# Kernel optimization log

Hardware: AMD Instinct MI355X
Metric: run time of the kernel (lower is better)

## Reference

```python
import jax, jax.numpy as jnp
import numpy as np

B, K, C = 512, 64, 2048  # batch, mixture components, copy (eval points)


def setup_inputs() -> dict:
    key = jax.random.key(0)
    kw, km, ks, kr, kx = jax.random.split(key, 5)
    w = jax.random.uniform(kw, (B, K), dtype=jnp.float32)            # mixture weights
    means = jax.random.normal(km, (B, K, 2), dtype=jnp.float32)      # mean1, mean2
    sds = jax.random.uniform(ks, (B, K, 2), dtype=jnp.float32,
                             minval=0.5, maxval=1.5)                 # sd1, sd2 (>0)
    corr = jax.random.uniform(kr, (B, K), dtype=jnp.float32,
                              minval=-0.8, maxval=0.8)               # |corr| < 1
    model_out = jnp.concatenate(
        [w[..., None], means, sds, corr[..., None]], axis=-1)        # [B, K, 6]
    X = jax.random.normal(kx, (B, C, 2), dtype=jnp.float32)
    return {"model_out": model_out, "X": X}


def reference(model_out, X):
    # Unpack params: w, mean1, mean2, sd1, sd2, corr  -- each [B, K]
    w = model_out[..., 0]
    m1 = model_out[..., 1]
    m2 = model_out[..., 2]
    s1 = model_out[..., 3]
    s2 = model_out[..., 4]
    r = model_out[..., 5]

    # Closed-form bivariate normal pdf (equivalent to Cholesky-based
    # MultivariateNormal log_prob for the 2x2 covariance built in torch).
    # dx, dy: [B, C, K] via broadcasting X[B,C,1] against params[B,1,K]
    dx = (X[:, :, 0:1] - m1[:, None, :]) / s1[:, None, :]
    dy = (X[:, :, 1:2] - m2[:, None, :]) / s2[:, None, :]
    rb = r[:, None, :]
    omr2 = 1.0 - rb * rb  # 1 - rho^2
    z = dx * dx - 2.0 * rb * dx * dy + dy * dy
    two_pi = 2.0 * jnp.pi
    norm = two_pi * s1[:, None, :] * s2[:, None, :] * jnp.sqrt(omr2)
    probs = jnp.exp(-0.5 * z / omr2) / norm  # [B, C, K]

    # Weighted sum over components -> [B, C]
    return jnp.einsum('bck,bk->bc', probs, w)
```

## Files before the change

### kernel.cpp

```cpp
#include <hip/hip_runtime.h>
#include <hip/hip_bf16.h>


typedef float v2f __attribute__((ext_vector_type(2)));

constexpr int B = 512;
constexpr int K = 64;
constexpr int C = 2048;
constexpr int BLOCK = 256;
constexpr int HALVES = 2;
constexpr int CH = C / HALVES;

__global__ __launch_bounds__(BLOCK, 4) void mixture_kernel(
    const float* __restrict__ mo,
    const float* __restrict__ X,
    float* __restrict__ out)
{
    __shared__ float4 P[K][2];

    const int bid = blockIdx.x;
    const int b   = bid >> 1;
    const int h   = bid & 1;
    const int t   = threadIdx.x;

    if (t < K) {
        const float* p = mo + ((size_t)(b * K + t)) * 6;
        const float w  = p[0];
        const float m1 = p[1];
        const float m2 = p[2];
        const float s1 = p[3];
        const float s2 = p[4];
        const float r  = p[5];

        const float omr2 = fmaf(-r, r, 1.0f);
        const float inv  = 1.0f / omr2;
        const float a2   = 0.7213475204444817f * inv;
        const float sc   = sqrtf(a2);
        const float is1  = sc / s1;
        const float is2  = sc / s2;
        const float wn   = w * 0.15915494309189535f / (s1 * s2 * sqrtf(omr2));

        P[t][0] = make_float4(is1, is2, m1 * is1, m2 * is2);
        P[t][1] = make_float4(2.0f * r, wn, 0.0f, 0.0f);
    }
    __syncthreads();

    const float4* Xb = (const float4*)(X + (size_t)b * C * 2 + (size_t)h * CH * 2);
    const float4 xv0 = Xb[t];
    const float4 xv1 = Xb[t + BLOCK];

    v2f xs[2] = { {xv0.x, xv0.z}, {xv1.x, xv1.z} };
    v2f ys[2] = { {xv0.y, xv0.w}, {xv1.y, xv1.w} };
    v2f acc[2] = { {0.0f, 0.0f}, {0.0f, 0.0f} };

#pragma unroll 4
    for (int k = 0; k < K; ++k) {
        const float4 p0 = P[k][0];
        const float4 p1 = P[k][1];
        const v2f vis1 = { p0.x, p0.x };
        const v2f vis2 = { p0.y, p0.y };
        const v2f vnm1 = { -p0.z, -p0.z };
        const v2f vnm2 = { -p0.w, -p0.w };
        const v2f v2r  = { p1.x, p1.x };
        const v2f vwn  = { p1.y, p1.y };
#pragma unroll
        for (int j = 0; j < 2; ++j) {
            const v2f dx = __builtin_elementwise_fma(xs[j], vis1, vnm1);
            const v2f dy = __builtin_elementwise_fma(ys[j], vis2, vnm2);
            const v2f pq = dx * dy;
            v2f u        = dx * dx;
            u            = __builtin_elementwise_fma(dy, dy, u);
            const v2f e  = __builtin_elementwise_fma(v2r, pq, -u);
            v2f ex;
            ex.x = __builtin_amdgcn_exp2f(e.x);
            ex.y = __builtin_amdgcn_exp2f(e.y);
            acc[j] = __builtin_elementwise_fma(vwn, ex, acc[j]);
        }
    }

    float2* ob = (float2*)(out + (size_t)b * C + (size_t)h * CH);
    ob[t]         = make_float2(acc[0].x, acc[0].y);
    ob[t + BLOCK] = make_float2(acc[1].x, acc[1].y);
}

extern "C" void kernel_launch(void* const* d_in, const int* in_sizes, int n_in,
                              void* d_out, int out_size, void* d_ws, size_t ws_size,
                              hipStream_t stream) {
    const float* mo = (const float*)d_in[0];
    const float* X  = (const float*)d_in[1];
    float* out      = (float*)d_out;

    mixture_kernel<<<dim3(B * HALVES), dim3(BLOCK), 0, stream>>>(mo, X, out);
}
```

Baseline: 72.35 us.

## Split parameter preprocessing into separate prep kernel with pre-broadcast layout

```diff
diff --git a/kernel.cpp b/kernel.cpp
--- a/kernel.cpp
+++ b/kernel.cpp
@@ -11,76 +11,97 @@
 constexpr int HALVES = 2;
 constexpr int CH = C / HALVES;
 
-__global__ __launch_bounds__(BLOCK, 4) void mixture_kernel(
+__global__ __launch_bounds__(256) void prep_kernel(
     const float* __restrict__ mo,
+    float* __restrict__ P)
+{
+    const int i = blockIdx.x * 256 + threadIdx.x;
+    const float* p = mo + (size_t)i * 6;
+    const float w  = p[0];
+    const float m1 = p[1];
+    const float m2 = p[2];
+    const float s1 = p[3];
+    const float s2 = p[4];
+    const float r  = p[5];
+
+    const float omr2 = fmaf(-r, r, 1.0f);
+    const float inv  = 1.0f / omr2;
+    const float a2   = 0.7213475204444817f * inv;
+    const float sc   = sqrtf(a2);
+    const float is1  = sc / s1;
+    const float is2  = sc / s2;
+    const float nm1  = -(m1 * is1);
+    const float nm2  = -(m2 * is2);
+    const float r2   = 2.0f * r;
+    const float wn   = w * 0.15915494309189535f / (s1 * s2 * sqrtf(omr2));
+
+    float4* q = (float4*)(P + (size_t)i * 16);
+    q[0] = make_float4(is1, is1, is2, is2);
+    q[1] = make_float4(nm1, nm1, nm2, nm2);
+    q[2] = make_float4(r2, r2, wn, wn);
+}
+
+__global__ __launch_bounds__(BLOCK) void mixture_kernel(
     const float* __restrict__ X,
+    const float* __restrict__ P,
     float* __restrict__ out)
 {
-    __shared__ float4 P[K][2];
-
     const int bid = blockIdx.x;
     const int b   = bid >> 1;
     const int h   = bid & 1;
     const int t   = threadIdx.x;
 
-    if (t < K) {
-        const float* p = mo + ((size_t)(b * K + t)) * 6;
-        const float w  = p[0];
-        const float m1 = p[1];
-        const float m2 = p[2];
-        const float s1 = p[3];
-        const float s2 = p[4];
-        const float r  = p[5];
-
-        const float omr2 = fmaf(-r, r, 1.0f);
-        const float inv  = 1.0f / omr2;
-        const float a2   = 0.7213475204444817f * inv;
-        const float sc   = sqrtf(a2);
-        const float is1  = sc / s1;
-        const float is2  = sc / s2;
-        const float wn   = w * 0.15915494309189535f / (s1 * s2 * sqrtf(omr2));
-
-        P[t][0] = make_float4(is1, is2, m1 * is1, m2 * is2);
-        P[t][1] = make_float4(2.0f * r, wn, 0.0f, 0.0f);
-    }
-    __syncthreads();
-
     const float4* Xb = (const float4*)(X + (size_t)b * C * 2 + (size_t)h * CH * 2);
     const float4 xv0 = Xb[t];
     const float4 xv1 = Xb[t + BLOCK];
 
-    v2f xs[2] = { {xv0.x, xv0.z}, {xv1.x, xv1.z} };
-    v2f ys[2] = { {xv0.y, xv0.w}, {xv1.y, xv1.w} };
-    v2f acc[2] = { {0.0f, 0.0f}, {0.0f, 0.0f} };
+    const v2f xs0 = { xv0.x, xv0.z };
+    const v2f ys0 = { xv0.y, xv0.w };
+    const v2f xs1 = { xv1.x, xv1.z };
+    const v2f ys1 = { xv1.y, xv1.w };
+    v2f acc0 = { 0.0f, 0.0f };
+    v2f acc1 = { 0.0f, 0.0f };
+
+    const v2f* __restrict__ Pb = (const v2f*)(P + (size_t)b * K * 16);
 
 #pragma unroll 4
     for (int k = 0; k < K; ++k) {
-        const float4 p0 = P[k][0];
-        const float4 p1 = P[k][1];
-        const v2f vis1 = { p0.x, p0.x };
-        const v2f vis2 = { p0.y, p0.y };
-        const v2f vnm1 = { -p0.z, -p0.z };
-        const v2f vnm2 = { -p0.w, -p0.w };
-        const v2f v2r  = { p1.x, p1.x };
-        const v2f vwn  = { p1.y, p1.y };
-#pragma unroll
-        for (int j = 0; j < 2; ++j) {
-            const v2f dx = __builtin_elementwise_fma(xs[j], vis1, vnm1);
-            const v2f dy = __builtin_elementwise_fma(ys[j], vis2, vnm2);
+        const v2f IS1 = Pb[k * 8 + 0];
+        const v2f IS2 = Pb[k * 8 + 1];
+        const v2f NM1 = Pb[k * 8 + 2];
+        const v2f NM2 = Pb[k * 8 + 3];
+        const v2f R2  = Pb[k * 8 + 4];
+        const v2f WN  = Pb[k * 8 + 5];
+
+        {
+            const v2f dx = __builtin_elementwise_fma(xs0, IS1, NM1);
+            const v2f dy = __builtin_elementwise_fma(ys0, IS2, NM2);
             const v2f pq = dx * dy;
             v2f u        = dx * dx;
             u            = __builtin_elementwise_fma(dy, dy, u);
-            const v2f e  = __builtin_elementwise_fma(v2r, pq, -u);
+            const v2f e  = __builtin_elementwise_fma(R2, pq, -u);
             v2f ex;
             ex.x = __builtin_amdgcn_exp2f(e.x);
             ex.y = __builtin_amdgcn_exp2f(e.y);
-            acc[j] = __builtin_elementwise_fma(vwn, ex, acc[j]);
+            acc0 = __builtin_elementwise_fma(WN, ex, acc0);
+        }
+        {
+            const v2f dx = __builtin_elementwise_fma(xs1, IS1, NM1);
+            const v2f dy = __builtin_elementwise_fma(ys1, IS2, NM2);
+            const v2f pq = dx * dy;
+            v2f u        = dx * dx;
+            u            = __builtin_elementwise_fma(dy, dy, u);
+            const v2f e  = __builtin_elementwise_fma(R2, pq, -u);
+            v2f ex;
+            ex.x = __builtin_amdgcn_exp2f(e.x);
+            ex.y = __builtin_amdgcn_exp2f(e.y);
+            acc1 = __builtin_elementwise_fma(WN, ex, acc1);
         }
     }
 
     float2* ob = (float2*)(out + (size_t)b * C + (size_t)h * CH);
-    ob[t]         = make_float2(acc[0].x, acc[0].y);
-    ob[t + BLOCK] = make_float2(acc[1].x, acc[1].y);
+    ob[t]         = make_float2(acc0.x, acc0.y);
+    ob[t + BLOCK] = make_float2(acc1.x, acc1.y);
 }
 
 extern "C" void kernel_launch(void* const* d_in, const int* in_sizes, int n_in,
@@ -89,6 +110,8 @@
     const float* mo = (const float*)d_in[0];
     const float* X  = (const float*)d_in[1];
     float* out      = (float*)d_out;
+    float* P        = (float*)d_ws;
 
-    mixture_kernel<<<dim3(B * HALVES), dim3(BLOCK), 0, stream>>>(mo, X, out);
+    prep_kernel<<<dim3(B * K / 256), dim3(256), 0, stream>>>(mo, P);
+    mixture_kernel<<<dim3(B * HALVES), dim3(BLOCK), 0, stream>>>(X, P, out);
 }
```

After: 79.64 us. 1.1x slower.

## Expand quadratic form into per-component coefficients and fold weight into exponent

Applied to the files above, without the earlier changes.

```diff
diff --git a/kernel.cpp b/kernel.cpp
--- a/kernel.cpp
+++ b/kernel.cpp
@@ -1,5 +1,4 @@
 #include <hip/hip_runtime.h>
-#include <hip/hip_bf16.h>
 
 
 typedef float v2f __attribute__((ext_vector_type(2)));
@@ -16,7 +15,7 @@
     const float* __restrict__ X,
     float* __restrict__ out)
 {
-    __shared__ float4 P[K][2];
+    __shared__ float4 P[K][3];
 
     const int bid = blockIdx.x;
     const int b   = bid >> 1;
@@ -24,24 +23,34 @@
     const int t   = threadIdx.x;
 
     if (t < K) {
-        const float* p = mo + ((size_t)(b * K + t)) * 6;
-        const float w  = p[0];
-        const float m1 = p[1];
-        const float m2 = p[2];
-        const float s1 = p[3];
-        const float s2 = p[4];
-        const float r  = p[5];
+        const float* p6 = mo + ((size_t)(b * K + t)) * 6;
+        const float w  = p6[0];
+        const float m1 = p6[1];
+        const float m2 = p6[2];
+        const float s1 = p6[3];
+        const float s2 = p6[4];
+        const float r  = p6[5];
 
         const float omr2 = fmaf(-r, r, 1.0f);
         const float inv  = 1.0f / omr2;
-        const float a2   = 0.7213475204444817f * inv;
-        const float sc   = sqrtf(a2);
-        const float is1  = sc / s1;
-        const float is2  = sc / s2;
-        const float wn   = w * 0.15915494309189535f / (s1 * s2 * sqrtf(omr2));
+        const float g    = 0.7213475204444817f * inv;
+        const float i1   = 1.0f / s1;
+        const float i2   = 1.0f / s2;
+        const float p    = g * i1 * i1;
+        const float q    = g * i2 * i2;
+        const float s    = 2.0f * r * g * i1 * i2;
+        const float A    = -p;
+        const float Bc   = -q;
+        const float Cc   = s;
+        const float D    = fmaf(2.0f * p, m1, -s * m2);
+        const float E    = fmaf(2.0f * q, m2, -s * m1);
+        const float wn   = w * 0.15915494309189535f * i1 * i2 * sqrtf(inv);
+        const float L    = log2f(fmaxf(wn, 1e-37f));
+        const float F    = fmaf(-p, m1 * m1, fmaf(-q, m2 * m2, fmaf(s, m1 * m2, L)));
 
-        P[t][0] = make_float4(is1, is2, m1 * is1, m2 * is2);
-        P[t][1] = make_float4(2.0f * r, wn, 0.0f, 0.0f);
+        P[t][0] = make_float4(A, A, Bc, Bc);
+        P[t][1] = make_float4(Cc, Cc, D, D);
+        P[t][2] = make_float4(E, E, F, F);
     }
     __syncthreads();
 
@@ -49,32 +58,36 @@
     const float4 xv0 = Xb[t];
     const float4 xv1 = Xb[t + BLOCK];
 
-    v2f xs[2] = { {xv0.x, xv0.z}, {xv1.x, xv1.z} };
-    v2f ys[2] = { {xv0.y, xv0.w}, {xv1.y, xv1.w} };
+    const v2f xp[2]  = { {xv0.x, xv0.z}, {xv1.x, xv1.z} };
+    const v2f yp[2]  = { {xv0.y, xv0.w}, {xv1.y, xv1.w} };
+    const v2f xx[2]  = { xp[0] * xp[0], xp[1] * xp[1] };
+    const v2f yy[2]  = { yp[0] * yp[0], yp[1] * yp[1] };
+    const v2f xy[2]  = { xp[0] * yp[0], xp[1] * yp[1] };
     v2f acc[2] = { {0.0f, 0.0f}, {0.0f, 0.0f} };
 
 #pragma unroll 4
     for (int k = 0; k < K; ++k) {
-        const float4 p0 = P[k][0];
-        const float4 p1 = P[k][1];
-        const v2f vis1 = { p0.x, p0.x };
-        const v2f vis2 = { p0.y, p0.y };
-        const v2f vnm1 = { -p0.z, -p0.z };
-        const v2f vnm2 = { -p0.w, -p0.w };
-        const v2f v2r  = { p1.x, p1.x };
-        const v2f vwn  = { p1.y, p1.y };
+        const float4 c0 = P[k][0];
+        const float4 c1 = P[k][1];
+        const float4 c2 = P[k][2];
+        const v2f A2 = { c0.x, c0.y };
+        const v2f B2 = { c0.z, c0.w };
+        const v2f C2 = { c1.x, c1.y };
+        const v2f D2 = { c1.z, c1.w };
+        const v2f E2 = { c2.x, c2.y };
+        const v2f F2 = { c2.z, c2.w };
+
 #pragma unroll
         for (int j = 0; j < 2; ++j) {
-            const v2f dx = __builtin_elementwise_fma(xs[j], vis1, vnm1);
-            const v2f dy = __builtin_elementwise_fma(ys[j], vis2, vnm2);
-            const v2f pq = dx * dy;
-            v2f u        = dx * dx;
-            u            = __builtin_elementwise_fma(dy, dy, u);
-            const v2f e  = __builtin_elementwise_fma(v2r, pq, -u);
+            v2f e = __builtin_elementwise_fma(A2, xx[j], F2);
+            e     = __builtin_elementwise_fma(B2, yy[j], e);
+            e     = __builtin_elementwise_fma(C2, xy[j], e);
+            e     = __builtin_elementwise_fma(D2, xp[j], e);
+            e     = __builtin_elementwise_fma(E2, yp[j], e);
             v2f ex;
             ex.x = __builtin_amdgcn_exp2f(e.x);
             ex.y = __builtin_amdgcn_exp2f(e.y);
-            acc[j] = __builtin_elementwise_fma(vwn, ex, acc[j]);
+            acc[j] = acc[j] + ex;
         }
     }
 
```

Measured after the change: 71.57 us. About the same (-1.1%).
